# Optimization experiments

Hardware: AMD Instinct MI355X
Metric: run time of the kernel (lower is better)

Reference implementation:

```python
import math
import jax, jax.numpy as jnp
import numpy as np

B, T, C, H = 2, 2048, 1024, 16
HD = C // H
ALPHA = 32.0


def setup_inputs() -> dict:
    key = jax.random.key(0)
    ks = jax.random.split(key, 16)
    s = 0.02
    inp = {
        "query": jax.random.normal(ks[0], (B, T, C), jnp.float32),
        "key": jax.random.normal(ks[1], (B, T, C), jnp.float32),
        "value": jax.random.normal(ks[2], (B, T, C), jnp.float32),
        # causal mask: 0 => masked (matches masked_fill(att_mask == 0, -inf))
        "att_mask": jnp.tril(jnp.ones((1, 1, T, T), jnp.float32)),
        "Wq": jax.random.normal(ks[3], (C, C), jnp.float32) * s,
        "bq": jnp.zeros((C,), jnp.float32),
        "Wk": jax.random.normal(ks[4], (C, C), jnp.float32) * s,
        "bk": jnp.zeros((C,), jnp.float32),
        "Wv": jax.random.normal(ks[5], (C, C), jnp.float32) * s,
        "bv": jnp.zeros((C,), jnp.float32),
        "Wp": jax.random.normal(ks[6], (C, C), jnp.float32) * s,
        "bp": jnp.zeros((C,), jnp.float32),
    }
    return inp


def reference(query, key, value, att_mask, Wq, bq, Wk, bk, Wv, bv, Wp, bp):
    b, tq, c = query.shape
    tk = key.shape[1]
    # separate QKV projections, split heads: [B,H,T,HD]
    q = (query @ Wq + bq).reshape(b, tq, H, HD).transpose(0, 2, 1, 3)
    k = (key @ Wk + bk).reshape(b, tk, H, HD).transpose(0, 2, 1, 3)
    v = (value @ Wv + bv).reshape(b, tk, H, HD).transpose(0, 2, 1, 3)
    # PBrelax: pre-scale q by 1/(alpha*sqrt(hd)), subtract detached global abs-max, rescale
    att = jnp.einsum("bhqd,bhkd->bhqk", q * (1.0 / ALPHA / math.sqrt(HD)), k)
    att = (att - jax.lax.stop_gradient(jnp.max(jnp.abs(att)))) * ALPHA
    att = jnp.where(att_mask[:, :, :tq, :tk] == 0, -jnp.inf, att)
    att = jax.nn.softmax(att, axis=-1)
    y = jnp.einsum("bhqk,bhkd->bhqd", att, v)
    y = y.transpose(0, 2, 1, 3).reshape(b, tq, c)
    return y @ Wp + bp
```

## Files before the change

### kernel.cpp

```cpp
#include <hip/hip_runtime.h>


#define Bsz 2
#define Tsz 2048
#define Csz 1024
#define Hsz 16
#define HDsz 64

typedef __bf16 bf16;
typedef __bf16 bf16x8 __attribute__((ext_vector_type(8)));
typedef __bf16 bf16x4 __attribute__((ext_vector_type(4)));
typedef float float4v __attribute__((ext_vector_type(4)));

#define MFMA16(a, b, c) __builtin_amdgcn_mfma_f32_16x16x32_bf16(a, b, c, 0, 0, 0)

#define GLOAD_LDS16(gptr, lptr)                                      \
  __builtin_amdgcn_global_load_lds(                                  \
      (const __attribute__((address_space(1))) void*)(gptr),         \
      (__attribute__((address_space(3))) void*)(lptr), 16, 0, 0)

__global__ __launch_bounds__(256) void cast3_bf16(
    const float* __restrict__ q, const float* __restrict__ k,
    const float* __restrict__ v, bf16* __restrict__ oq,
    bf16* __restrict__ ok, bf16* __restrict__ ov) {
  const int z = blockIdx.z;
  const float* src = z == 0 ? q : (z == 1 ? k : v);
  bf16* dst = z == 0 ? oq : (z == 1 ? ok : ov);
  const size_t i = ((size_t)blockIdx.x * 256 + threadIdx.x) * 8;
  const float4 a = *(const float4*)(src + i);
  const float4 b = *(const float4*)(src + i + 4);
  bf16x8 o;
  o[0] = (bf16)a.x; o[1] = (bf16)a.y; o[2] = (bf16)a.z; o[3] = (bf16)a.w;
  o[4] = (bf16)b.x; o[5] = (bf16)b.y; o[6] = (bf16)b.z; o[7] = (bf16)b.w;
  *(bf16x8*)(dst + i) = o;
}

__global__ __launch_bounds__(256) void wtrans_bf16(
    const float* __restrict__ Wq, const float* __restrict__ Wk,
    const float* __restrict__ Wv, const float* __restrict__ Wp,
    bf16* __restrict__ WT) {
  const int z = blockIdx.z;
  const float* W = z == 0 ? Wq : (z == 1 ? Wk : (z == 2 ? Wv : Wp));
  bf16* out = WT + (size_t)z * (Csz * Csz);
  __shared__ float Ts[64][68];
  const int k0 = blockIdx.y * 64, n0 = blockIdx.x * 64;
  const int tid = threadIdx.x;
#pragma unroll
  for (int it = 0; it < 4; ++it) {
    const int idx = it * 256 + tid;
    const int r = idx >> 4, c4 = (idx & 15) * 4;
    *(float4*)&Ts[r][c4] = *(const float4*)(W + (size_t)(k0 + r) * Csz + n0 + c4);
  }
  __syncthreads();
#pragma unroll
  for (int it = 0; it < 2; ++it) {
    const int idx = it * 256 + tid;
    const int n = idx & 63, k8 = (idx >> 6) * 8;
    bf16x8 o;
#pragma unroll
    for (int j = 0; j < 8; ++j) o[j] = (bf16)Ts[k8 + j][n];
    *(bf16x8*)(out + (size_t)(n0 + n) * Csz + k0 + k8) = o;
  }
}

__global__ __launch_bounds__(512, 2) void gemm256_qkv(
    const bf16* __restrict__ A0, const bf16* __restrict__ A1,
    const bf16* __restrict__ A2, const bf16* __restrict__ Wt,
    const float* __restrict__ b0, const float* __restrict__ b1,
    const float* __restrict__ b2, bf16* __restrict__ C0,
    bf16* __restrict__ C1, bf16* __restrict__ Vt) {
  constexpr int NT = Csz / 64;
  const int z = blockIdx.z;
  const bf16* A = z == 0 ? A0 : (z == 1 ? A1 : A2);
  const float* bias = z == 0 ? b0 : (z == 1 ? b1 : b2);
  const bf16* Bt = Wt + (size_t)z * (Csz * Csz);
  const int m0 = blockIdx.y * 256;
  const int nz0 = blockIdx.x * 256;

  __shared__ bf16 As[2 * 256 * 64];
  __shared__ bf16 Bs[2 * 256 * 64];

  const int tid = threadIdx.x;
  const int wave = tid >> 6, lane = tid & 63;
  const int l15 = lane & 15, quad = lane >> 4;
  const int wm = wave >> 2, wn = wave & 3;

  const int srow = tid >> 3;
  const int sch = tid & 7;
  const bf16* Ab = A + (size_t)(m0 + srow) * Csz + (sch ^ (srow & 7)) * 8;
  const bf16* Bb = Bt + (size_t)(nz0 + srow) * Csz + (sch ^ (srow & 7)) * 8;

#define STG(Xb, lds, lbuf, hh, tt)                                           \
  {                                                                          \
    GLOAD_LDS16((Xb) + (size_t)((hh)*128) * Csz + (size_t)(tt)*64,           \
                &(lds)[(lbuf) * (256 * 64) + (hh)*8192 + tid * 8]);          \
    GLOAD_LDS16((Xb) + (size_t)((hh)*128 + 64) * Csz + (size_t)(tt)*64,     \
                &(lds)[(lbuf) * (256 * 64) + (hh)*8192 + 4096 + tid * 8]);  \
  }
#define RD_A(dst, lbuf, i2, ks)                                              \
  dst = *(const bf16x8*)&As[(lbuf) * (256 * 64) +                            \
                            (wm * 128 + (i2)*16 + l15) * 64 +                \
                            ((((ks)*4 + quad) ^ (l15 & 7)) * 8)];
#define RD_B(dst, lbuf, j2, ks)                                              \
  dst = *(const bf16x8*)&Bs[(lbuf) * (256 * 64) +                            \
                            (wn * 64 + (j2)*16 + l15) * 64 +                 \
                            ((((ks)*4 + quad) ^ (l15 & 7)) * 8)];

  float4v acc[8][4];
#pragma unroll
  for (int i = 0; i < 8; ++i)
#pragma unroll
    for (int j = 0; j < 4; ++j) acc[i][j] = (float4v){0.f, 0.f, 0.f, 0.f};

  STG(Ab, As, 0, 0, 0);
  STG(Ab, As, 0, 1, 0);
  STG(Bb, Bs, 0, 0, 0);
  STG(Bb, Bs, 0, 1, 0);
  STG(Ab, As, 1, 0, 1);
  STG(Ab, As, 1, 1, 1);
  asm volatile("s_waitcnt vmcnt(4)" ::: "memory");
  __builtin_amdgcn_s_barrier();
  __builtin_amdgcn_sched_barrier(0);

#pragma unroll 1
  for (int t = 0; t < NT; ++t) {
    const int bsel = t & 1;
    bf16x8 af0[4][2], af1[4][2], bf0[2][2], bf1[2][2];

#pragma unroll
    for (int i = 0; i < 4; ++i) {
      RD_A(af0[i][0], bsel, i, 0);
      RD_A(af0[i][1], bsel, i, 1);
    }
#pragma unroll
    for (int j = 0; j < 2; ++j) {
      RD_B(bf0[j][0], bsel, j, 0);
      RD_B(bf0[j][1], bsel, j, 1);
    }
    if (t + 1 < NT) STG(Bb, Bs, bsel ^ 1, 0, t + 1);
    __builtin_amdgcn_s_barrier();
    asm volatile("s_waitcnt lgkmcnt(0)" ::: "memory");
    __builtin_amdgcn_sched_barrier(0);
    __builtin_amdgcn_s_setprio(1);
#pragma unroll
    for (int i = 0; i < 4; ++i)
#pragma unroll
      for (int j = 0; j < 2; ++j) {
        acc[i][j] = MFMA16(af0[i][0], bf0[j][0], acc[i][j]);
        acc[i][j] = MFMA16(af0[i][1], bf0[j][1], acc[i][j]);
      }
    __builtin_amdgcn_s_setprio(0);
    __builtin_amdgcn_s_barrier();

#pragma unroll
    for (int i = 0; i < 4; ++i) {
      RD_A(af1[i][0], bsel, 4 + i, 0);
      RD_A(af1[i][1], bsel, 4 + i, 1);
    }
    if (t + 1 < NT) STG(Bb, Bs, bsel ^ 1, 1, t + 1);
    __builtin_amdgcn_s_barrier();
    asm volatile("s_waitcnt lgkmcnt(0)" ::: "memory");
    __builtin_amdgcn_sched_barrier(0);
    __builtin_amdgcn_s_setprio(1);
#pragma unroll
    for (int i = 0; i < 4; ++i)
#pragma unroll
      for (int j = 0; j < 2; ++j) {
        acc[4 + i][j] = MFMA16(af1[i][0], bf0[j][0], acc[4 + i][j]);
        acc[4 + i][j] = MFMA16(af1[i][1], bf0[j][1], acc[4 + i][j]);
      }
    __builtin_amdgcn_s_setprio(0);
    __builtin_amdgcn_s_barrier();

#pragma unroll
    for (int j = 0; j < 2; ++j) {
      RD_B(bf1[j][0], bsel, 2 + j, 0);
      RD_B(bf1[j][1], bsel, 2 + j, 1);
    }
    if (t + 2 < NT) STG(Ab, As, bsel, 0, t + 2);
    __builtin_amdgcn_s_barrier();
    asm volatile("s_waitcnt lgkmcnt(0)" ::: "memory");
    __builtin_amdgcn_sched_barrier(0);
    __builtin_amdgcn_s_setprio(1);
#pragma unroll
    for (int i = 0; i < 4; ++i)
#pragma unroll
      for (int j = 0; j < 2; ++j) {
        acc[i][2 + j] = MFMA16(af0[i][0], bf1[j][0], acc[i][2 + j]);
        acc[i][2 + j] = MFMA16(af0[i][1], bf1[j][1], acc[i][2 + j]);
      }
    __builtin_amdgcn_s_setprio(0);
    __builtin_amdgcn_s_barrier();

    if (t + 2 < NT) STG(Ab, As, bsel, 1, t + 2);
    __builtin_amdgcn_s_barrier();
    __builtin_amdgcn_s_setprio(1);
#pragma unroll
    for (int i = 0; i < 4; ++i)
#pragma unroll
      for (int j = 0; j < 2; ++j) {
        acc[4 + i][2 + j] = MFMA16(af1[i][0], bf1[j][0], acc[4 + i][2 + j]);
        acc[4 + i][2 + j] = MFMA16(af1[i][1], bf1[j][1], acc[4 + i][2 + j]);
      }
    __builtin_amdgcn_s_setprio(0);
    if (t + 2 < NT) {
      asm volatile("s_waitcnt vmcnt(4)" ::: "memory");
    } else if (t + 1 < NT) {
      asm volatile("s_waitcnt vmcnt(0)" ::: "memory");
    }
    __builtin_amdgcn_s_barrier();
    __builtin_amdgcn_sched_barrier(0);
  }
#undef STG
#undef RD_A
#undef RD_B

  const int omb0 = m0 + wm * 128 + quad * 4;
  const int onb0 = nz0 + wn * 64 + l15;
  if (z == 2) {
#pragma unroll
    for (int j = 0; j < 4; ++j) {
      const int n = onb0 + j * 16;
      const float bj = bias[n];
#pragma unroll
      for (int i = 0; i < 8; ++i) {
        const int mrow = omb0 + i * 16;
        const int bb = mrow >> 11, tt = mrow & (Tsz - 1);
        union { bf16 h[4]; uint2 u; } pk;
#pragma unroll
        for (int r = 0; r < 4; ++r) pk.h[r] = (bf16)(acc[i][j][r] + bj);
        *(uint2*)(Vt + ((size_t)(bb * 1024 + n)) * Tsz + tt) = pk.u;
      }
    }
  } else {
    bf16* C = z == 0 ? C0 : C1;
    const float osc = z == 0 ? 0.180336880111124f : 1.0f;
#pragma unroll
    for (int j = 0; j < 4; ++j) {
      const float bj = bias[onb0 + j * 16];
#pragma unroll
      for (int i = 0; i < 8; ++i) {
#pragma unroll
        for (int r = 0; r < 4; ++r) {
          const float v = (acc[i][j][r] + bj) * osc;
          C[(size_t)(omb0 + i * 16 + r) * Csz + onb0 + j * 16] = (bf16)v;
        }
      }
    }
  }
}

template <typename OutT, bool VTR>
__global__ __launch_bounds__(256) void gemm_mfma(
    const bf16* __restrict__ A0, const bf16* __restrict__ A1,
    const bf16* __restrict__ A2, const bf16* __restrict__ Wt,
    const float* __restrict__ b0, const float* __restrict__ b1,
    const float* __restrict__ b2, OutT* __restrict__ C0,
    OutT* __restrict__ C1, OutT* __restrict__ C2, int M, int N, int K) {
  const int z = blockIdx.z;
  const bf16* A = z == 0 ? A0 : (z == 1 ? A1 : A2);
  const float* bias = z == 0 ? b0 : (z == 1 ? b1 : b2);
  OutT* C = z == 0 ? C0 : (z == 1 ? C1 : C2);
  const bf16* Bt = Wt + (size_t)z * N * K;
  const float osc = (VTR && z == 0) ? 0.180336880111124f : 1.0f;

  __shared__ bf16 As[128 * 32];
  __shared__ bf16 Bs[128 * 32];
  const int tid = threadIdx.x;
  const int wave = tid >> 6, lane = tid & 63;
  const int l15 = lane & 15, quad = lane >> 4;
  const int m0 = blockIdx.y * 128, n0 = blockIdx.x * 128;
  const int wm = (wave >> 1) * 64, wn = (wave & 1) * 64;
  const int srow = tid >> 2, schunk = tid & 3;

  float4v acc[4][4];
#pragma unroll
  for (int i = 0; i < 4; ++i)
#pragma unroll
    for (int j = 0; j < 4; ++j) acc[i][j] = (float4v){0.f, 0.f, 0.f, 0.f};

  for (int k0 = 0; k0 < K; k0 += 32) {
    __syncthreads();
#pragma unroll
    for (int p = 0; p < 2; ++p) {
      const int row = p * 64 + srow;
      GLOAD_LDS16(A + (size_t)(m0 + row) * K + k0 + schunk * 8,
                  &As[(p * 256 + tid) * 8]);
      GLOAD_LDS16(Bt + (size_t)(n0 + row) * K + k0 + schunk * 8,
                  &Bs[(p * 256 + tid) * 8]);
    }
    __syncthreads();

    bf16x8 af[4], bfr[4];
#pragma unroll
    for (int i = 0; i < 4; ++i)
      af[i] = *(const bf16x8*)&As[(wm + i * 16 + l15) * 32 + quad * 8];
#pragma unroll
    for (int j = 0; j < 4; ++j)
      bfr[j] = *(const bf16x8*)&Bs[(wn + j * 16 + l15) * 32 + quad * 8];
#pragma unroll
    for (int i = 0; i < 4; ++i)
#pragma unroll
      for (int j = 0; j < 4; ++j)
        acc[i][j] = MFMA16(af[i], bfr[j], acc[i][j]);
  }

  const int omb = m0 + wm + quad * 4;
  const int onb = n0 + wn + l15;
  if (VTR && z == 2) {
#pragma unroll
    for (int j = 0; j < 4; ++j) {
      const int n = onb + j * 16;
      const float bj = bias[n];
#pragma unroll
      for (int i = 0; i < 4; ++i) {
        const int mrow = omb + i * 16;
        const int bb = mrow >> 11, t = mrow & (Tsz - 1);
        union { bf16 h[4]; uint2 u; } pk;
#pragma unroll
        for (int r = 0; r < 4; ++r) pk.h[r] = (bf16)(acc[i][j][r] + bj);
        *(uint2*)((bf16*)C + ((size_t)(bb * 1024 + n)) * Tsz + t) = pk.u;
      }
    }
  } else {
#pragma unroll
    for (int j = 0; j < 4; ++j) {
      const float bj = bias[onb + j * 16];
#pragma unroll
      for (int i = 0; i < 4; ++i) {
#pragma unroll
        for (int r = 0; r < 4; ++r) {
          const float v = (acc[i][j][r] + bj) * osc;
          const size_t off = (size_t)(omb + i * 16 + r) * N + onb + j * 16;
          if constexpr (sizeof(OutT) == 2)
            C[off] = (OutT)v;
          else
            C[off] = v;
        }
      }
    }
  }
}

__global__ __launch_bounds__(256) void attn_mfma(const bf16* __restrict__ Q,
                                                 const bf16* __restrict__ K,
                                                 const bf16* __restrict__ Vt,
                                                 bf16* __restrict__ Y) {
  __shared__ bf16 Ks[3][64 * 64];
  __shared__ bf16 Vs[3][64 * 64];
  __shared__ bf16 Ps[4][32 * 72];

  const int bh = blockIdx.y;
  const int b = bh >> 4, h = bh & 15;
  int xr = (blockIdx.x & 1) ? (int)(gridDim.x - 1 - (blockIdx.x >> 1))
                            : (int)(blockIdx.x >> 1);
  if (bh >= 16) xr = (int)(gridDim.x - 1) - xr;
  const int i0 = xr * 128;
  const int tid = threadIdx.x;
  const int wave = tid >> 6, lane = tid & 63;
  const int l15 = lane & 15, quad = lane >> 4;

  const int srow = tid >> 3;
  const int sch = tid & 7;

  const bf16* kb = K + (size_t)b * Tsz * Csz + h * HDsz;
  const bf16* vb = Vt + (size_t)bh * HDsz * Tsz;

  const int qb = i0 + wave * 32;

  bf16x8 qf[2][2];
#pragma unroll
  for (int sub = 0; sub < 2; ++sub) {
    const bf16* qp =
        Q + ((size_t)(b * Tsz + qb + sub * 16 + l15)) * Csz + h * HDsz + quad * 8;
    qf[sub][0] = *(const bf16x8*)qp;
    qf[sub][1] = *(const bf16x8*)(qp + 32);
  }

  bf16x8 ones;
#pragma unroll
  for (int j = 0; j < 8; ++j) ones[j] = (bf16)1.0f;

  float4v Of[2][4];
  float4v accl[2];
#pragma unroll
  for (int sub = 0; sub < 2; ++sub) {
    accl[sub] = (float4v){0.f, 0.f, 0.f, 0.f};
#pragma unroll
    for (int nc = 0; nc < 4; ++nc) Of[sub][nc] = (float4v){0.f, 0.f, 0.f, 0.f};
  }

  const int ntile = i0 / 64 + 2;

#define STAGE_KV(tt, bb)                                                     \
  {                                                                          \
    _Pragma("unroll") for (int p = 0; p < 2; ++p) {                          \
      const int r = p * 32 + srow;                                           \
      const int c = sch ^ (r & 7);                                           \
      GLOAD_LDS16(kb + (size_t)((tt)*64 + r) * Csz + c * 8,                  \
                  &Ks[bb][(p * 256 + tid) * 8]);                             \
      GLOAD_LDS16(vb + (size_t)r * Tsz + (tt)*64 + c * 8,                    \
                  &Vs[bb][(p * 256 + tid) * 8]);                             \
    }                                                                        \
  }

  STAGE_KV(0, 0);
  STAGE_KV(1, 1);
  asm volatile("s_waitcnt vmcnt(4)" ::: "memory");
  __builtin_amdgcn_s_barrier();
  __builtin_amdgcn_sched_barrier(0);

  int bcur = 0;
#pragma unroll 1
  for (int t = 0; t < ntile; ++t) {
    const int j0 = t * 64;
    const int bst = bcur == 0 ? 2 : bcur - 1;
    if (t + 2 < ntile) STAGE_KV(t + 2, bst);

    if (j0 <= qb + 31) {
      float4v S[2][4];
#pragma unroll
      for (int nc = 0; nc < 4; ++nc) {
        const int row = nc * 16 + l15;
        const bf16x8 k0 =
            *(const bf16x8*)&Ks[bcur][row * 64 + ((quad ^ (row & 7)) * 8)];
        const bf16x8 k1 =
            *(const bf16x8*)&Ks[bcur][row * 64 + (((quad + 4) ^ (row & 7)) * 8)];
#pragma unroll
        for (int sub = 0; sub < 2; ++sub) {
          float4v a = (float4v){0.f, 0.f, 0.f, 0.f};
          a = MFMA16(k0, qf[sub][0], a);
          a = MFMA16(k1, qf[sub][1], a);
          S[sub][nc] = a;
        }
      }

      if (j0 + 63 > qb) {
#pragma unroll
        for (int sub = 0; sub < 2; ++sub) {
          const int q = qb + sub * 16 + l15;
#pragma unroll
          for (int nc = 0; nc < 4; ++nc) {
            const int keyb = j0 + nc * 16 + quad * 4;
#pragma unroll
            for (int r = 0; r < 4; ++r)
              if (keyb + r > q) S[sub][nc][r] = -1e30f;
          }
        }
      }

#pragma unroll
      for (int sub = 0; sub < 2; ++sub) {
#pragma unroll
        for (int nc = 0; nc < 4; ++nc) {
          bf16x4 pk;
#pragma unroll
          for (int r = 0; r < 4; ++r)
            pk[r] = (bf16)__builtin_amdgcn_exp2f(S[sub][nc][r]);
          *(bf16x4*)&Ps[wave][(sub * 16 + l15) * 72 + nc * 16 + quad * 4] = pk;
        }
      }

      bf16x8 pf[2][2];
#pragma unroll
      for (int sub = 0; sub < 2; ++sub) {
#pragma unroll
        for (int kc = 0; kc < 2; ++kc)
          pf[sub][kc] = *(const bf16x8*)
              &Ps[wave][(sub * 16 + l15) * 72 + kc * 32 + quad * 8];
        accl[sub] = MFMA16(ones, pf[sub][0], accl[sub]);
        accl[sub] = MFMA16(ones, pf[sub][1], accl[sub]);
      }
#pragma unroll
      for (int nc = 0; nc < 4; ++nc) {
        const int row = nc * 16 + l15;
#pragma unroll
        for (int kc = 0; kc < 2; ++kc) {
          const bf16x8 vf = *(const bf16x8*)
              &Vs[bcur][row * 64 + (((kc * 4 + quad) ^ (row & 7)) * 8)];
#pragma unroll
          for (int sub = 0; sub < 2; ++sub)
            Of[sub][nc] = MFMA16(vf, pf[sub][kc], Of[sub][nc]);
        }
      }
    }

    if (t + 2 < ntile) {
      asm volatile("s_waitcnt vmcnt(4)" ::: "memory");
    } else if (t + 1 < ntile) {
      asm volatile("s_waitcnt vmcnt(0)" ::: "memory");
    }
    __builtin_amdgcn_sched_barrier(0);
    __builtin_amdgcn_s_barrier();
    __builtin_amdgcn_sched_barrier(0);
    bcur = bcur == 2 ? 0 : bcur + 1;
  }
#undef STAGE_KV

#pragma unroll
  for (int sub = 0; sub < 2; ++sub) {
    const float rl = __builtin_amdgcn_rcpf(accl[sub][0]);
    const size_t rowoff =
        ((size_t)(b * Tsz + qb + sub * 16 + l15)) * Csz + h * HDsz;
#pragma unroll
    for (int nc = 0; nc < 4; ++nc) {
      union { bf16 h4[4]; uint2 u; } pk;
#pragma unroll
      for (int r = 0; r < 4; ++r) pk.h4[r] = (bf16)(Of[sub][nc][r] * rl);
      *(uint2*)(Y + rowoff + nc * 16 + quad * 4) = pk.u;
    }
  }
}

extern "C" void kernel_launch(void* const* d_in, const int* in_sizes, int n_in,
                              void* d_out, int out_size, void* d_ws,
                              size_t ws_size, hipStream_t stream) {
  const float* query = (const float*)d_in[0];
  const float* key = (const float*)d_in[1];
  const float* value = (const float*)d_in[2];
  const float* Wq = (const float*)d_in[4];
  const float* bq = (const float*)d_in[5];
  const float* Wk = (const float*)d_in[6];
  const float* bk = (const float*)d_in[7];
  const float* Wv = (const float*)d_in[8];
  const float* bv = (const float*)d_in[9];
  const float* Wp = (const float*)d_in[10];
  const float* bp = (const float*)d_in[11];
  float* out = (float*)d_out;

  char* ws = (char*)d_ws;
  bf16* WT = (bf16*)(ws);
  bf16* vc = (bf16*)(ws + (8u << 20));
  bf16* Qp = (bf16*)(ws + (16u << 20));
  bf16* Kp = (bf16*)(ws + (24u << 20));
  bf16* Vt = (bf16*)(ws + (32u << 20));
  bf16* Yb = vc;
  bf16* qc = (bf16*)d_out;
  bf16* kc = (bf16*)((char*)d_out + (8u << 20));

  const int M = Bsz * Tsz;

  cast3_bf16<<<dim3((M * Csz) / (256 * 8), 1, 3), dim3(256), 0, stream>>>(
      query, key, value, qc, kc, vc);
  wtrans_bf16<<<dim3(16, 16, 4), dim3(256), 0, stream>>>(Wq, Wk, Wv, Wp, WT);
  gemm256_qkv<<<dim3(Csz / 256, M / 256, 3), dim3(512), 0, stream>>>(
      qc, kc, vc, WT, bq, bk, bv, Qp, Kp, Vt);
  attn_mfma<<<dim3(Tsz / 128, Bsz * Hsz), dim3(256), 0, stream>>>(Qp, Kp, Vt,
                                                                  Yb);
  gemm_mfma<float, false><<<dim3(Csz / 128, M / 128, 1), dim3(256), 0, stream>>>(
      Yb, Yb, Yb, WT + 3u * (Csz * Csz), bp, bp, bp, out, out, out, M, Csz,
      Csz);
}
```

Baseline: 248.7 us.

## Software-pipeline attention loop: overlap PV MFMAs of previous tile with QK of current

```diff
diff --git a/kernel.cpp b/kernel.cpp
--- a/kernel.cpp
+++ b/kernel.cpp
@@ -352,9 +352,7 @@
 
   const int bh = blockIdx.y;
   const int b = bh >> 4, h = bh & 15;
-  int xr = (blockIdx.x & 1) ? (int)(gridDim.x - 1 - (blockIdx.x >> 1))
-                            : (int)(blockIdx.x >> 1);
-  if (bh >= 16) xr = (int)(gridDim.x - 1) - xr;
+  const int xr = (((int)blockIdx.x & 7) << 1) | ((int)blockIdx.x >> 3);
   const int i0 = xr * 128;
   const int tid = threadIdx.x;
   const int wave = tid >> 6, lane = tid & 63;
@@ -367,6 +365,8 @@
   const bf16* vb = Vt + (size_t)bh * HDsz * Tsz;
 
   const int qb = i0 + wave * 32;
+  const int lastT = (qb + 31) >> 6;
+  const int ntile = i0 / 64 + 2;
 
   bf16x8 qf[2][2];
 #pragma unroll
@@ -389,8 +389,6 @@
 #pragma unroll
     for (int nc = 0; nc < 4; ++nc) Of[sub][nc] = (float4v){0.f, 0.f, 0.f, 0.f};
   }
-
-  const int ntile = i0 / 64 + 2;
 
 #define STAGE_KV(tt, bb)                                                     \
   {                                                                          \
@@ -404,98 +402,115 @@
     }                                                                        \
   }
 
+  bf16x8 vf[2][4][2];
+  bf16x8 pf[2][2][2];
+
   STAGE_KV(0, 0);
   STAGE_KV(1, 1);
   asm volatile("s_waitcnt vmcnt(4)" ::: "memory");
   __builtin_amdgcn_s_barrier();
   __builtin_amdgcn_sched_barrier(0);
 
+#define ATTN_BODY(T_, SL_)                                                   \
+  {                                                                          \
+    const int t_ = (T_);                                                     \
+    const int j0_ = t_ * 64;                                                 \
+    const int bst_ = bcur == 0 ? 2 : bcur - 1;                               \
+    if (t_ + 2 < ntile) STAGE_KV(t_ + 2, bst_);                              \
+    const bool act_ = (t_ <= lastT);                                         \
+    if (act_) {                                                              \
+      _Pragma("unroll") for (int nc = 0; nc < 4; ++nc) {                     \
+        const int row = nc * 16 + l15;                                       \
+        _Pragma("unroll") for (int kc = 0; kc < 2; ++kc)                     \
+            vf[SL_][nc][kc] = *(const bf16x8*)&Vs[bcur]                      \
+                [row * 64 + (((kc * 4 + quad) ^ (row & 7)) * 8)];            \
+      }                                                                      \
+      float4v S[2][4];                                                       \
+      _Pragma("unroll") for (int nc = 0; nc < 4; ++nc) {                     \
+        const int row = nc * 16 + l15;                                       \
+        const bf16x8 k0 = *(const bf16x8*)&Ks[bcur]                          \
+            [row * 64 + ((quad ^ (row & 7)) * 8)];                           \
+        const bf16x8 k1 = *(const bf16x8*)&Ks[bcur]                          \
+            [row * 64 + (((quad + 4) ^ (row & 7)) * 8)];                     \
+        _Pragma("unroll") for (int sub = 0; sub < 2; ++sub) {                \
+          float4v a = (float4v){0.f, 0.f, 0.f, 0.f};                         \
+          a = MFMA16(k0, qf[sub][0], a);                                     \
+          a = MFMA16(k1, qf[sub][1], a);                                     \
+          S[sub][nc] = a;                                                    \
+        }                                                                    \
+      }                                                                      \
+      if (j0_ + 63 > qb) {                                                   \
+        _Pragma("unroll") for (int sub = 0; sub < 2; ++sub) {                \
+          const int q = qb + sub * 16 + l15;                                 \
+          _Pragma("unroll") for (int nc = 0; nc < 4; ++nc) {                 \
+            const int keyb = j0_ + nc * 16 + quad * 4;                       \
+            _Pragma("unroll") for (int r = 0; r < 4; ++r)                    \
+                if (keyb + r > q) S[sub][nc][r] = -1e30f;                    \
+          }                                                                  \
+        }                                                                    \
+      }                                                                      \
+      _Pragma("unroll") for (int sub = 0; sub < 2; ++sub) {                  \
+        _Pragma("unroll") for (int nc = 0; nc < 4; ++nc) {                   \
+          bf16x4 pk;                                                         \
+          _Pragma("unroll") for (int r = 0; r < 4; ++r)                      \
+              pk[r] = (bf16)__builtin_amdgcn_exp2f(S[sub][nc][r]);           \
+          *(bf16x4*)&Ps[wave][(sub * 16 + l15) * 72 + nc * 16 + quad * 4] =  \
+              pk;                                                            \
+        }                                                                    \
+      }                                                                      \
+    }                                                                        \
+    if (t_ >= 1 && t_ - 1 <= lastT) {                                        \
+      _Pragma("unroll") for (int sub = 0; sub < 2; ++sub) {                  \
+        accl[sub] = MFMA16(ones, pf[SL_ ^ 1][sub][0], accl[sub]);            \
+        accl[sub] = MFMA16(ones, pf[SL_ ^ 1][sub][1], accl[sub]);            \
+      }                                                                      \
+      _Pragma("unroll") for (int nc = 0; nc < 4; ++nc)                       \
+          _Pragma("unroll") for (int kc = 0; kc < 2; ++kc)                   \
+              _Pragma("unroll") for (int sub = 0; sub < 2; ++sub)            \
+                  Of[sub][nc] = MFMA16(vf[SL_ ^ 1][nc][kc],                  \
+                                       pf[SL_ ^ 1][sub][kc], Of[sub][nc]);   \
+    }                                                                        \
+    if (act_) {                                                              \
+      _Pragma("unroll") for (int sub = 0; sub < 2; ++sub)                    \
+          _Pragma("unroll") for (int kc = 0; kc < 2; ++kc)                   \
+              pf[SL_][sub][kc] = *(const bf16x8*)                            \
+                  &Ps[wave][(sub * 16 + l15) * 72 + kc * 32 + quad * 8];     \
+    }                                                                        \
+    if (t_ + 2 < ntile) {                                                    \
+      asm volatile("s_waitcnt vmcnt(4)" ::: "memory");                       \
+    } else if (t_ + 1 < ntile) {                                             \
+      asm volatile("s_waitcnt vmcnt(0)" ::: "memory");                       \
+    }                                                                        \
+    asm volatile("s_waitcnt lgkmcnt(0)" ::: "memory");                       \
+    __builtin_amdgcn_sched_barrier(0);                                       \
+    __builtin_amdgcn_s_barrier();                                            \
+    __builtin_amdgcn_sched_barrier(0);                                       \
+    bcur = bcur == 2 ? 0 : bcur + 1;                                         \
+  }
+
   int bcur = 0;
 #pragma unroll 1
-  for (int t = 0; t < ntile; ++t) {
-    const int j0 = t * 64;
-    const int bst = bcur == 0 ? 2 : bcur - 1;
-    if (t + 2 < ntile) STAGE_KV(t + 2, bst);
-
-    if (j0 <= qb + 31) {
-      float4v S[2][4];
-#pragma unroll
-      for (int nc = 0; nc < 4; ++nc) {
-        const int row = nc * 16 + l15;
-        const bf16x8 k0 =
-            *(const bf16x8*)&Ks[bcur][row * 64 + ((quad ^ (row & 7)) * 8)];
-        const bf16x8 k1 =
-            *(const bf16x8*)&Ks[bcur][row * 64 + (((quad + 4) ^ (row & 7)) * 8)];
-#pragma unroll
-        for (int sub = 0; sub < 2; ++sub) {
-          float4v a = (float4v){0.f, 0.f, 0.f, 0.f};
-          a = MFMA16(k0, qf[sub][0], a);
-          a = MFMA16(k1, qf[sub][1], a);
-          S[sub][nc] = a;
-        }
-      }
-
-      if (j0 + 63 > qb) {
-#pragma unroll
-        for (int sub = 0; sub < 2; ++sub) {
-          const int q = qb + sub * 16 + l15;
-#pragma unroll
-          for (int nc = 0; nc < 4; ++nc) {
-            const int keyb = j0 + nc * 16 + quad * 4;
-#pragma unroll
-            for (int r = 0; r < 4; ++r)
-              if (keyb + r > q) S[sub][nc][r] = -1e30f;
-          }
-        }
-      }
-
-#pragma unroll
-      for (int sub = 0; sub < 2; ++sub) {
-#pragma unroll
-        for (int nc = 0; nc < 4; ++nc) {
-          bf16x4 pk;
-#pragma unroll
-          for (int r = 0; r < 4; ++r)
-            pk[r] = (bf16)__builtin_amdgcn_exp2f(S[sub][nc][r]);
-          *(bf16x4*)&Ps[wave][(sub * 16 + l15) * 72 + nc * 16 + quad * 4] = pk;
-        }
-      }
-
-      bf16x8 pf[2][2];
-#pragma unroll
-      for (int sub = 0; sub < 2; ++sub) {
-#pragma unroll
-        for (int kc = 0; kc < 2; ++kc)
-          pf[sub][kc] = *(const bf16x8*)
-              &Ps[wave][(sub * 16 + l15) * 72 + kc * 32 + quad * 8];
-        accl[sub] = MFMA16(ones, pf[sub][0], accl[sub]);
-        accl[sub] = MFMA16(ones, pf[sub][1], accl[sub]);
-      }
-#pragma unroll
-      for (int nc = 0; nc < 4; ++nc) {
-        const int row = nc * 16 + l15;
-#pragma unroll
-        for (int kc = 0; kc < 2; ++kc) {
-          const bf16x8 vf = *(const bf16x8*)
-              &Vs[bcur][row * 64 + (((kc * 4 + quad) ^ (row & 7)) * 8)];
-#pragma unroll
-          for (int sub = 0; sub < 2; ++sub)
-            Of[sub][nc] = MFMA16(vf, pf[sub][kc], Of[sub][nc]);
-        }
-      }
-    }
-
-    if (t + 2 < ntile) {
-      asm volatile("s_waitcnt vmcnt(4)" ::: "memory");
-    } else if (t + 1 < ntile) {
-      asm volatile("s_waitcnt vmcnt(0)" ::: "memory");
-    }
-    __builtin_amdgcn_sched_barrier(0);
-    __builtin_amdgcn_s_barrier();
-    __builtin_amdgcn_sched_barrier(0);
-    bcur = bcur == 2 ? 0 : bcur + 1;
-  }
+  for (int tt = 0; tt < ntile; tt += 2) {
+    ATTN_BODY(tt, 0);
+    ATTN_BODY(tt + 1, 1);
+  }
+#undef ATTN_BODY
 #undef STAGE_KV
+
+  if (lastT == ntile - 1) {
+#pragma unroll
+    for (int sub = 0; sub < 2; ++sub) {
+      accl[sub] = MFMA16(ones, pf[1][sub][0], accl[sub]);
+      accl[sub] = MFMA16(ones, pf[1][sub][1], accl[sub]);
+    }
+#pragma unroll
+    for (int nc = 0; nc < 4; ++nc)
+#pragma unroll
+      for (int kc = 0; kc < 2; ++kc)
+#pragma unroll
+        for (int sub = 0; sub < 2; ++sub)
+          Of[sub][nc] = MFMA16(vf[1][nc][kc], pf[1][sub][kc], Of[sub][nc]);
+  }
 
 #pragma unroll
   for (int sub = 0; sub < 2; ++sub) {
```

Result: slower. 281.8 us (+13.3%).
